# Kernel tuning notes

Measured on AMD Instinct MI355X. Metric: run time of the kernel, lower is better.

Reference implementation:

```python
import jax, jax.numpy as jnp
import numpy as np

KNN = 5
SEARCH = 3
CUTOFF = 1.0
NCLASSES = 21
D, H, W = 32, 128, 2048
P = 1048576


def setup_inputs() -> dict:
    key = jax.random.key(0)
    k1, k2, k3, k4, k5, k6 = jax.random.split(key, 6)
    proj_range = jax.random.uniform(k1, (D, H, W), dtype=jnp.float32)
    unproj_range = jax.random.uniform(k2, (P,), dtype=jnp.float32)
    proj_argmax = jax.random.randint(k3, (D, H, W), 0, NCLASSES).astype(jnp.int32)
    px = jax.random.randint(k4, (P,), 0, W).astype(jnp.int32)
    py = jax.random.randint(k5, (P,), 0, H).astype(jnp.int32)
    pz = jax.random.randint(k6, (P,), 0, D).astype(jnp.int32)
    return {"proj_range": proj_range, "unproj_range": unproj_range,
            "proj_argmax": proj_argmax, "px": px, "py": py, "pz": pz}


def reference(proj_range, unproj_range, proj_argmax, px, py, pz):
    pad = (SEARCH - 1) // 2
    k3 = SEARCH ** 3
    center = (k3 - 1) // 2  # = 13 for search=3
    n_pts = unproj_range.shape[0]

    # zero padding replicates F.unfold's implicit zero pad (padded entries stay 0,
    # which is NOT mapped to inf by the `< 0` mask, matching the torch code)
    pr_pad = jnp.pad(proj_range, pad)
    pa_pad = jnp.pad(proj_argmax, pad)

    # kernel offsets, flattened in (dz, dy, dx) order like unfoldNd
    offs = jnp.arange(SEARCH, dtype=jnp.int32)
    oz, oy, ox = jnp.meshgrid(offs, offs, offs, indexing="ij")
    oz, oy, ox = oz.reshape(-1), oy.reshape(-1), ox.reshape(-1)  # [k3]

    # per-point neighborhood indices into the padded volume: [P, k3]
    zi = pz[:, None] + oz[None, :]
    yi = py[:, None] + oy[None, :]
    xi = px[:, None] + ox[None, :]

    nb_rang = pr_pad[zi, yi, xi]                       # [P, k3]
    nb_rang = jnp.where(nb_rang < 0, jnp.inf, nb_rang)
    nb_rang = nb_rang.at[:, center].set(unproj_range)  # center = query range

    k2_dist = jnp.abs(nb_rang - unproj_range[:, None])  # [P, k3]

    neg_top, knn_idx = jax.lax.top_k(-k2_dist, KNN)     # smallest-k distances
    knn_dist = -neg_top                                  # [P, KNN]

    nb_arg = pa_pad[zi, yi, xi]                          # [P, k3] int
    knn_arg = jnp.take_along_axis(nb_arg, knn_idx, axis=1)
    knn_arg = jnp.where(knn_dist > CUTOFF, NCLASSES, knn_arg)  # cutoff -> invalid class

    # scatter-add voting over classes 0..NCLASSES
    counts = jnp.zeros((n_pts, NCLASSES + 1), dtype=proj_range.dtype)
    counts = counts.at[jnp.arange(n_pts, dtype=jnp.int32)[:, None], knn_arg].add(1.0)

    # argmax over classes 1..NCLASSES-1 (drop class 0 and invalid bucket), then +1
    out = jnp.argmax(counts[:, 1:-1], axis=1).astype(jnp.int32) + 1
    return out
```

## Files before the change

kernel.cpp:

```cpp
#include <hip/hip_runtime.h>
#include <math.h>

#define KNN 5
#define K3 27
#define CENTER 13
#define NCLASSES 21
#define DIM_D 32
#define DIM_H 128
#define DIM_W 2048

#define RADIX 256
#define BIN_PTS 2048
#define SEG_TILE 2048


typedef float    float4u __attribute__((ext_vector_type(4), aligned(4)));
typedef int      int4u   __attribute__((ext_vector_type(4), aligned(4)));
typedef unsigned uint4u  __attribute__((ext_vector_type(4), aligned(4)));

#define SENTINEL 3.0e38f
#define BITS_TWO 0x4000000000000000ULL
#define M_SCALE 8388608.0f

__device__ __forceinline__ unsigned seg_of_xy(int x, int y) {
    return ((unsigned)y << 1) | ((unsigned)x >> 10);
}
__device__ __forceinline__ unsigned seg_of_wy(unsigned wy) {
    return (((wy >> 11) & 0x7Fu) << 1) | ((wy >> 10) & 1u);
}
__device__ __forceinline__ unsigned b8_of_wy(unsigned wy) {
    return (((wy >> 18) & 31u) << 3) | ((wy >> 7) & 7u);
}

__global__ __launch_bounds__(256) void pack_hist_kernel(
    const float4* __restrict__ pr4, const int4* __restrict__ pa4,
    uint4* __restrict__ cv4,
    const int* __restrict__ px, const int* __restrict__ py,
    unsigned* __restrict__ partial, int n4, int P, int chunk)
{
    __shared__ unsigned lh0[RADIX];
    int t = threadIdx.x, b = blockIdx.x;

    int i = b * 256 + t;
    if (i < n4) {
        float4 v = pr4[i];
        int4   c = pa4[i];
        uint4 w;
        w.x = ((unsigned)(v.x * M_SCALE) << 5) | ((unsigned)c.x & 31u);
        w.y = ((unsigned)(v.y * M_SCALE) << 5) | ((unsigned)c.y & 31u);
        w.z = ((unsigned)(v.z * M_SCALE) << 5) | ((unsigned)c.z & 31u);
        w.w = ((unsigned)(v.w * M_SCALE) << 5) | ((unsigned)c.w & 31u);
        cv4[i] = w;
    }

    if (b < RADIX) {
        lh0[t] = 0;
        __syncthreads();
        int start = b * chunk;
        int end = min(P, start + chunk);
        for (int i0 = start + t * 4; i0 < end; i0 += 256 * 4) {
            if (i0 + 3 < end) {
                int i4 = i0 >> 2;
                int4 X = ((const int4*)px)[i4];
                int4 Y = ((const int4*)py)[i4];
                atomicAdd(&lh0[seg_of_xy(X.x, Y.x)], 1u);
                atomicAdd(&lh0[seg_of_xy(X.y, Y.y)], 1u);
                atomicAdd(&lh0[seg_of_xy(X.z, Y.z)], 1u);
                atomicAdd(&lh0[seg_of_xy(X.w, Y.w)], 1u);
            } else {
                for (int j = i0; j < end; ++j)
                    atomicAdd(&lh0[seg_of_xy(px[j], py[j])], 1u);
            }
        }
        __syncthreads();
        partial[b * RADIX + t] = lh0[t];
    }
}

__global__ __launch_bounds__(256) void scan_reduce_kernel(
    const unsigned* __restrict__ partial, unsigned* __restrict__ g0,
    unsigned* __restrict__ hbase)
{
    __shared__ unsigned ws[4];
    int t = threadIdx.x, lane = t & 63, wid = t >> 6;
    unsigned a = 0;
    for (int b = 0; b < RADIX; ++b)
        a += partial[b * RADIX + t];
    unsigned ia = a;
#pragma unroll
    for (int off = 1; off < 64; off <<= 1) {
        unsigned v = __shfl_up(ia, off);
        if (lane >= off) ia += v;
    }
    if (lane == 63) ws[wid] = ia;
    __syncthreads();
    unsigned b = 0;
#pragma unroll
    for (int w = 0; w < 4; ++w) b += (w < wid) ? ws[w] : 0u;
    unsigned excl = b + ia - a;
    g0[t] = excl;
    hbase[t] = excl;
}

struct BinShared {
    unsigned lh[RADIX];
    unsigned lscan[RADIX];
    unsigned gbase[RADIX];
    unsigned wsum[4];
    unsigned stW[BIN_PTS];
    unsigned stU[BIN_PTS];
    unsigned stI[BIN_PTS];
};

__global__ __launch_bounds__(512) void bin_pass1_kernel(
    const float* __restrict__ ur, const int* __restrict__ px,
    const int* __restrict__ py, const int* __restrict__ pz,
    unsigned* __restrict__ g0,
    unsigned* __restrict__ oW, unsigned* __restrict__ oU,
    unsigned* __restrict__ oI, int P)
{
    __shared__ BinShared S;
    int t = threadIdx.x, lane = t & 63, wid = t >> 6;
    int bstart = blockIdx.x * BIN_PTS;
    int n = min(BIN_PTS, P - bstart);
    if (t < RADIX) S.lh[t] = 0;
    __syncthreads();

    unsigned pw[4], pu[4], rk[4], dg[4];
    {
        int i4 = (bstart >> 2) + t;
        int i0 = i4 * 4;
        if (i0 + 3 < P) {
            int4 X = ((const int4*)px)[i4];
            int4 Y = ((const int4*)py)[i4];
            int4 Z = ((const int4*)pz)[i4];
            float4 U = ((const float4*)ur)[i4];
            int xs[4] = {X.x, X.y, X.z, X.w};
            int ys[4] = {Y.x, Y.y, Y.z, Y.w};
            int zs[4] = {Z.x, Z.y, Z.z, Z.w};
            float us[4] = {U.x, U.y, U.z, U.w};
#pragma unroll
            for (int c = 0; c < 4; ++c) {
                dg[c] = seg_of_xy(xs[c], ys[c]);
                rk[c] = atomicAdd(&S.lh[dg[c]], 1u);
                pw[c] = (unsigned)xs[c] | ((unsigned)ys[c] << 11)
                        | ((unsigned)zs[c] << 18);
                pu[c] = (unsigned)(us[c] * M_SCALE);
            }
        } else {
#pragma unroll
            for (int c = 0; c < 4; ++c) {
                int gi = i0 + c;
                if (gi < P) {
                    int x = px[gi], y = py[gi], z = pz[gi];
                    dg[c] = seg_of_xy(x, y);
                    rk[c] = atomicAdd(&S.lh[dg[c]], 1u);
                    pw[c] = (unsigned)x | ((unsigned)y << 11)
                            | ((unsigned)z << 18);
                    pu[c] = (unsigned)(ur[gi] * M_SCALE);
                } else {
                    dg[c] = 0xFFFFFFFFu;
                }
            }
        }
    }
    __syncthreads();

    {
        unsigned c0 = (t < RADIX) ? S.lh[t] : 0u;
        unsigned inc = c0;
#pragma unroll
        for (int off = 1; off < 64; off <<= 1) {
            unsigned v = __shfl_up(inc, off);
            if (lane >= off) inc += v;
        }
        if (t < RADIX && lane == 63) S.wsum[wid] = inc;
        __syncthreads();
        if (t < RADIX) {
            unsigned wb = 0;
#pragma unroll
            for (int w = 0; w < 4; ++w) wb += (w < wid) ? S.wsum[w] : 0u;
            S.lscan[t] = wb + inc - c0;
            S.gbase[t] = c0 ? atomicAdd(&g0[t], c0) : 0u;
        }
    }
    __syncthreads();
#pragma unroll
    for (int c = 0; c < 4; ++c)
        if (dg[c] != 0xFFFFFFFFu) {
            unsigned sl = S.lscan[dg[c]] + rk[c];
            S.stW[sl] = pw[c];
            S.stU[sl] = pu[c];
            S.stI[sl] = (unsigned)(((bstart >> 2) + t) * 4 + c);
        }
    __syncthreads();
#pragma unroll
    for (int j = 0; j < 4; ++j) {
        int s = j * 512 + t;
        if (s < n) {
            unsigned wv = S.stW[s];
            unsigned d = seg_of_wy(wv);
            unsigned pos = S.gbase[d] + ((unsigned)s - S.lscan[d]);
            oW[pos] = wv;
            oU[pos] = S.stU[s];
            oI[pos] = S.stI[s];
        }
    }
}

__device__ __forceinline__ void bev_knn_body_u24(
    const unsigned* __restrict__ cv,
    unsigned mu, int x, int y, int z, int oidx, int* __restrict__ out)
{
    int xo = min(max(x - 1, 0), DIM_W - 4);
    int s = x - 1 - xo;

    uint4u Wv[9];
    bool okr[9];
#pragma unroll
    for (int r = 0; r < 9; ++r) {
        const int dz = r / 3 - 1;
        const int dy = r % 3 - 1;
        int zz = z + dz, yy = y + dy;
        bool ok = ((unsigned)zz < (unsigned)DIM_D) &
                  ((unsigned)yy < (unsigned)DIM_H);
        okr[r] = ok;
        int row = ok ? (zz * DIM_H + yy) : 0;
        Wv[r] = *(const uint4u*)(cv + (((size_t)row) << 11) + xo);
    }

    double bd[KNN];
#pragma unroll
    for (int j = 0; j < KNN; ++j) bd[j] = 1.0e308;

    auto push = [&](int k, unsigned w) {
        int diff = abs((int)(w >> 5) - (int)mu);
        if (k == CENTER) diff = 0;
        double kd = (double)diff * 1024.0
                  + (double)(((unsigned)k << 5) | (w & 31u));
#pragma unroll
        for (int j = 0; j < KNN; ++j) {
            double lo = fmin(bd[j], kd);
            kd = fmax(bd[j], kd);
            bd[j] = lo;
        }
    };

    bool fast = __all(s == 0);
    if (fast) {
#pragma unroll
        for (int r = 0; r < 9; ++r) {
            bool ok = okr[r];
            push(r * 3 + 0, ok ? Wv[r].x : 0u);
            push(r * 3 + 1, ok ? Wv[r].y : 0u);
            push(r * 3 + 2, ok ? Wv[r].z : 0u);
        }
    } else {
#pragma unroll
        for (int r = 0; r < 9; ++r) {
            bool ok = okr[r];
            unsigned a0 = ok ? Wv[r].x : 0u;
            unsigned a1 = ok ? Wv[r].y : 0u;
            unsigned a2 = ok ? Wv[r].z : 0u;
            unsigned a3 = ok ? Wv[r].w : 0u;
            unsigned w0 = (s == 0) ? a0 : ((s == -1) ? 0u : ((s == 1) ? a1 : a2));
            unsigned w1 = (s == 0) ? a1 : ((s == -1) ? a0 : ((s == 1) ? a2 : a3));
            unsigned w2 = (s == 0) ? a2 : ((s == -1) ? a1 : ((s == 1) ? a3 : 0u));
            push(r * 3 + 0, w0);
            push(r * 3 + 1, w1);
            push(r * 3 + 2, w2);
        }
    }

    int votes[KNN];
#pragma unroll
    for (int j = 0; j < KNN; ++j)
        votes[j] = (int)(((unsigned long long)bd[j]) & 31u);

    int best_cnt = 0, best_cls = 1;
#pragma unroll
    for (int j = 0; j < KNN; ++j) {
        int v = votes[j];
        if (v >= 1 && v <= NCLASSES - 1) {
            int cnt = 0;
#pragma unroll
            for (int i = 0; i < KNN; ++i) cnt += (votes[i] == v) ? 1 : 0;
            if (cnt > best_cnt || (cnt == best_cnt && v < best_cls)) {
                best_cnt = cnt;
                best_cls = v;
            }
        }
    }
    __builtin_nontemporal_store(best_cls, &out[oidx]);
}

__global__ __launch_bounds__(1024) void pass2_knn_kernel(
    const unsigned* __restrict__ iW, const unsigned* __restrict__ iU,
    const unsigned* __restrict__ iI, const unsigned* __restrict__ segBase,
    const unsigned* __restrict__ cv, int* __restrict__ out, int P)
{
    __shared__ unsigned lz[RADIX];
    __shared__ unsigned lsc[RADIX];
    __shared__ unsigned wsum[4];
    __shared__ unsigned stW[SEG_TILE];
    __shared__ unsigned stU[SEG_TILE];
    __shared__ unsigned stI[SEG_TILE];

    int bid = blockIdx.x;
    int b = bid >> 1, half = bid & 1;
    unsigned s0 = segBase[b];
    unsigned s1 = (b == RADIX - 1) ? (unsigned)P : segBase[b + 1];
    int t = threadIdx.x, lane = t & 63, wid = t >> 6;

    for (unsigned tb = s0 + (unsigned)half * SEG_TILE; tb < s1;
         tb += 2u * SEG_TILE) {
        unsigned m = min((unsigned)SEG_TILE, s1 - tb);
        if (t < RADIX) lz[t] = 0;
        __syncthreads();
        unsigned vw[2], vu[2], vi[2], rk[2], zz[2];
#pragma unroll
        for (int j = 0; j < 2; ++j) {
            int s = j * 1024 + t;
            if (s < (int)m) {
                unsigned gi = tb + (unsigned)s;
                vw[j] = iW[gi];
                vu[j] = iU[gi];
                vi[j] = iI[gi];
                zz[j] = b8_of_wy(vw[j]);
                rk[j] = atomicAdd(&lz[zz[j]], 1u);
            } else {
                zz[j] = 0xFFFFFFFFu;
            }
        }
        __syncthreads();
        {
            unsigned c0 = (t < RADIX) ? lz[t] : 0u;
            unsigned inc = c0;
#pragma unroll
            for (int off = 1; off < 64; off <<= 1) {
                unsigned v = __shfl_up(inc, off);
                if (lane >= off) inc += v;
            }
            if (t < RADIX && lane == 63) wsum[wid] = inc;
            __syncthreads();
            if (t < RADIX) {
                unsigned wb = 0;
#pragma unroll
                for (int w = 0; w < 4; ++w) wb += (w < wid) ? wsum[w] : 0u;
                lsc[t] = wb + inc - c0;
            }
        }
        __syncthreads();
#pragma unroll
        for (int j = 0; j < 2; ++j)
            if (zz[j] != 0xFFFFFFFFu) {
                unsigned sl = lsc[zz[j]] + rk[j];
                stW[sl] = vw[j];
                stU[sl] = vu[j];
                stI[sl] = vi[j];
            }
        __syncthreads();
#pragma unroll
        for (int j = 0; j < 2; ++j) {
            int sp = j * 1024 + t;
            if (sp < (int)m) {
                unsigned wv = stW[sp];
                int x = (int)(wv & 0x7FFu);
                int y = (int)((wv >> 11) & 0x7Fu);
                int z = (int)((wv >> 18) & 0x1Fu);
                bev_knn_body_u24(cv, stU[sp], x, y, z, (int)stI[sp], out);
            }
        }
        __syncthreads();
    }
}

__device__ __forceinline__ void bev_knn_body_gen(
    const float* __restrict__ pr, const int* __restrict__ pa,
    float u, int x, int y, int z, int oidx, int* __restrict__ out)
{
    int xo = min(max(x - 1, 0), DIM_W - 4);
    int s = x - 1 - xo;

    float4u L[9];
    int4u   A[9];
    bool okr[9];
#pragma unroll
    for (int r = 0; r < 9; ++r) {
        const int dz = r / 3 - 1;
        const int dy = r % 3 - 1;
        int zz = z + dz, yy = y + dy;
        bool ok = ((unsigned)zz < (unsigned)DIM_D) &
                  ((unsigned)yy < (unsigned)DIM_H);
        okr[r] = ok;
        int row = ok ? (zz * DIM_H + yy) : 0;
        size_t rb = ((size_t)row) << 11;
        L[r] = *(const float4u*)(pr + rb + xo);
        A[r] = *(const int4u*)(pa + rb + xo);
    }

    double bd[KNN];
#pragma unroll
    for (int j = 0; j < KNN; ++j) bd[j] = 1.0e308;

    auto push = [&](int k, float v, unsigned cls) {
        float d = fabsf(v - u);
        d = (v < 0.f) ? SENTINEL : d;
        if (k == CENTER) d = 0.0f;
        double key = (double)d + 1.0;
        unsigned long long kb =
            (unsigned long long)__double_as_longlong(key)
            | (unsigned long long)(((unsigned)k << 5) | (cls & 31u));
        double kd = __longlong_as_double((long long)kb);
#pragma unroll
        for (int j = 0; j < KNN; ++j) {
            double lo = fmin(bd[j], kd);
            kd = fmax(bd[j], kd);
            bd[j] = lo;
        }
    };

#pragma unroll
    for (int r = 0; r < 9; ++r) {
        bool ok = okr[r];
        float a0 = ok ? L[r].x : 0.f;
        float a1 = ok ? L[r].y : 0.f;
        float a2 = ok ? L[r].z : 0.f;
        float a3 = ok ? L[r].w : 0.f;
        float v0 = (s == 0) ? a0 : ((s == -1) ? 0.f : ((s == 1) ? a1 : a2));
        float v1 = (s == 0) ? a1 : ((s == -1) ? a0 : ((s == 1) ? a2 : a3));
        float v2 = (s == 0) ? a2 : ((s == -1) ? a1 : ((s == 1) ? a3 : 0.f));
        unsigned c0 = ok ? (unsigned)A[r].x : 0u;
        unsigned c1 = ok ? (unsigned)A[r].y : 0u;
        unsigned c2 = ok ? (unsigned)A[r].z : 0u;
        unsigned c3 = ok ? (unsigned)A[r].w : 0u;
        unsigned cv0 = (s == 0) ? c0 : ((s == -1) ? 0u : ((s == 1) ? c1 : c2));
        unsigned cv1 = (s == 0) ? c1 : ((s == -1) ? c0 : ((s == 1) ? c2 : c3));
        unsigned cv2 = (s == 0) ? c2 : ((s == -1) ? c1 : ((s == 1) ? c3 : 0u));
        push(r * 3 + 0, v0, cv0);
        push(r * 3 + 1, v1, cv1);
        push(r * 3 + 2, v2, cv2);
    }

    int votes[KNN];
#pragma unroll
    for (int j = 0; j < KNN; ++j) {
        unsigned long long kb =
            (unsigned long long)__double_as_longlong(bd[j]);
        int cls = (int)(kb & 31u);
        bool cut = (kb & ~1023ULL) > BITS_TWO;
        votes[j] = cut ? NCLASSES : cls;
    }

    int best_cnt = 0, best_cls = 1;
#pragma unroll
    for (int j = 0; j < KNN; ++j) {
        int v = votes[j];
        if (v >= 1 && v <= NCLASSES - 1) {
            int cnt = 0;
#pragma unroll
            for (int i = 0; i < KNN; ++i) cnt += (votes[i] == v) ? 1 : 0;
            if (cnt > best_cnt || (cnt == best_cnt && v < best_cls)) {
                best_cnt = cnt;
                best_cls = v;
            }
        }
    }
    out[oidx] = best_cls;
}

__global__ __launch_bounds__(256) void bev_knn_direct_kernel(
    const float* __restrict__ pr, const int* __restrict__ pa,
    const float* __restrict__ ur, const int* __restrict__ px,
    const int* __restrict__ py, const int* __restrict__ pz,
    int* __restrict__ out, int P)
{
    int p = blockIdx.x * blockDim.x + threadIdx.x;
    if (p >= P) return;
    bev_knn_body_gen(pr, pa, ur[p], px[p], py[p], pz[p], p, out);
}

extern "C" void kernel_launch(void* const* d_in, const int* in_sizes, int n_in,
                              void* d_out, int out_size, void* d_ws, size_t ws_size,
                              hipStream_t stream) {
    const float* pr = (const float*)d_in[0];
    const float* ur = (const float*)d_in[1];
    const int*   pa = (const int*)d_in[2];
    const int*   px = (const int*)d_in[3];
    const int*   py = (const int*)d_in[4];
    const int*   pz = (const int*)d_in[5];
    int* out = (int*)d_out;
    int P = in_sizes[1];
    int gridB = (P + BIN_PTS - 1) / BIN_PTS;
    int gridD = (P + 255) / 256;
    int chunk = (((P + RADIX - 1) / RADIX) + 3) & ~3;

    const int VOXELS = DIM_D * DIM_H * DIM_W;
    size_t g0_b   = (size_t)RADIX * 4;
    size_t hb_b   = (size_t)RADIX * 4;
    size_t part_b = (size_t)RADIX * RADIX * 4;
    size_t pre    = (g0_b + hb_b + part_b + 255) & ~(size_t)255;
    size_t arr_b  = ((size_t)P * 4 + 255) & ~(size_t)255;
    size_t cv_b   = ((size_t)VOXELS * 4 + 255) & ~(size_t)255;
    size_t need   = pre + 3 * arr_b + cv_b;

    if (ws_size >= need) {
        char* ws = (char*)d_ws;
        unsigned* g0     = (unsigned*)ws;
        unsigned* h0base = (unsigned*)(ws + g0_b);
        unsigned* part   = (unsigned*)(ws + g0_b + hb_b);
        unsigned* p1W = (unsigned*)(ws + pre);
        unsigned* p1U = (unsigned*)(ws + pre + arr_b);
        unsigned* p1I = (unsigned*)(ws + pre + 2 * arr_b);
        unsigned* cv  = (unsigned*)(ws + pre + 3 * arr_b);

        int n4 = VOXELS / 4;
        int gridP = max((n4 + 255) / 256, RADIX);
        pack_hist_kernel<<<gridP, 256, 0, stream>>>(
            (const float4*)pr, (const int4*)pa, (uint4*)cv,
            px, py, part, n4, P, chunk);
        scan_reduce_kernel<<<1, 256, 0, stream>>>(part, g0, h0base);
        bin_pass1_kernel<<<gridB, 512, 0, stream>>>(ur, px, py, pz, g0,
                                                    p1W, p1U, p1I, P);
        pass2_knn_kernel<<<2 * RADIX, 1024, 0, stream>>>(
            p1W, p1U, p1I, h0base, cv, out, P);
    } else {
        bev_knn_direct_kernel<<<gridD, 256, 0, stream>>>(pr, pa, ur, px, py,
                                                         pz, out, P);
    }
}
```

Baseline: 191.2 us.

## Split pass2 into fixed 1024-point windows with XCD-aware block swizzle

Pass 2 no longer has 512 blocks each looping over tiles of a variable-size segment. It now launches one block per fixed 1024-point window of the binned arrays, which removes the per-segment base array and balances load across blocks. A block-index swizzle spreads neighbouring windows across the 8 XCDs. Windows that straddle segment boundaries still get a local 8-bit radix sort, so sort locality may drop slightly at the edges, and each block now does a single small tile, which adds launch and sync overhead per point.

```diff
diff --git a/kernel.cpp b/kernel.cpp
--- a/kernel.cpp
+++ b/kernel.cpp
@@ -11,7 +11,7 @@
 
 #define RADIX 256
 #define BIN_PTS 2048
-#define SEG_TILE 2048
+#define WIN 1024
 
 
 typedef float    float4u __attribute__((ext_vector_type(4), aligned(4)));
@@ -78,8 +78,7 @@
 }
 
 __global__ __launch_bounds__(256) void scan_reduce_kernel(
-    const unsigned* __restrict__ partial, unsigned* __restrict__ g0,
-    unsigned* __restrict__ hbase)
+    const unsigned* __restrict__ partial, unsigned* __restrict__ g0)
 {
     __shared__ unsigned ws[4];
     int t = threadIdx.x, lane = t & 63, wid = t >> 6;
@@ -97,9 +96,7 @@
     unsigned b = 0;
 #pragma unroll
     for (int w = 0; w < 4; ++w) b += (w < wid) ? ws[w] : 0u;
-    unsigned excl = b + ia - a;
-    g0[t] = excl;
-    hbase[t] = excl;
+    g0[t] = b + ia - a;
 }
 
 struct BinShared {
@@ -294,84 +291,74 @@
     __builtin_nontemporal_store(best_cls, &out[oidx]);
 }
 
+__device__ __forceinline__ int swizzle_block(int b, int nb) {
+    if ((nb & 7) == 0) {
+        int per = nb >> 3;
+        return (b & 7) * per + (b >> 3);
+    }
+    return b;
+}
+
 __global__ __launch_bounds__(1024) void pass2_knn_kernel(
     const unsigned* __restrict__ iW, const unsigned* __restrict__ iU,
-    const unsigned* __restrict__ iI, const unsigned* __restrict__ segBase,
+    const unsigned* __restrict__ iI,
     const unsigned* __restrict__ cv, int* __restrict__ out, int P)
 {
     __shared__ unsigned lz[RADIX];
     __shared__ unsigned lsc[RADIX];
     __shared__ unsigned wsum[4];
-    __shared__ unsigned stW[SEG_TILE];
-    __shared__ unsigned stU[SEG_TILE];
-    __shared__ unsigned stI[SEG_TILE];
-
-    int bid = blockIdx.x;
-    int b = bid >> 1, half = bid & 1;
-    unsigned s0 = segBase[b];
-    unsigned s1 = (b == RADIX - 1) ? (unsigned)P : segBase[b + 1];
+    __shared__ unsigned stW[WIN];
+    __shared__ unsigned stU[WIN];
+    __shared__ unsigned stI[WIN];
+
+    int lb = swizzle_block(blockIdx.x, gridDim.x);
+    int base = lb * WIN;
+    int m = min(WIN, P - base);
     int t = threadIdx.x, lane = t & 63, wid = t >> 6;
 
-    for (unsigned tb = s0 + (unsigned)half * SEG_TILE; tb < s1;
-         tb += 2u * SEG_TILE) {
-        unsigned m = min((unsigned)SEG_TILE, s1 - tb);
-        if (t < RADIX) lz[t] = 0;
+    if (t < RADIX) lz[t] = 0;
+    __syncthreads();
+
+    unsigned vw = 0, vu = 0, vi = 0, rk = 0, zz = 0xFFFFFFFFu;
+    if (t < m) {
+        vw = iW[base + t];
+        vu = iU[base + t];
+        vi = iI[base + t];
+        zz = b8_of_wy(vw);
+        rk = atomicAdd(&lz[zz], 1u);
+    }
+    __syncthreads();
+    {
+        unsigned c0 = (t < RADIX) ? lz[t] : 0u;
+        unsigned inc = c0;
+#pragma unroll
+        for (int off = 1; off < 64; off <<= 1) {
+            unsigned v = __shfl_up(inc, off);
+            if (lane >= off) inc += v;
+        }
+        if (t < RADIX && lane == 63) wsum[wid] = inc;
         __syncthreads();
-        unsigned vw[2], vu[2], vi[2], rk[2], zz[2];
-#pragma unroll
-        for (int j = 0; j < 2; ++j) {
-            int s = j * 1024 + t;
-            if (s < (int)m) {
-                unsigned gi = tb + (unsigned)s;
-                vw[j] = iW[gi];
-                vu[j] = iU[gi];
-                vi[j] = iI[gi];
-                zz[j] = b8_of_wy(vw[j]);
-                rk[j] = atomicAdd(&lz[zz[j]], 1u);
-            } else {
-                zz[j] = 0xFFFFFFFFu;
-            }
-        }
-        __syncthreads();
-        {
-            unsigned c0 = (t < RADIX) ? lz[t] : 0u;
-            unsigned inc = c0;
-#pragma unroll
-            for (int off = 1; off < 64; off <<= 1) {
-                unsigned v = __shfl_up(inc, off);
-                if (lane >= off) inc += v;
-            }
-            if (t < RADIX && lane == 63) wsum[wid] = inc;
-            __syncthreads();
-            if (t < RADIX) {
-                unsigned wb = 0;
-#pragma unroll
-                for (int w = 0; w < 4; ++w) wb += (w < wid) ? wsum[w] : 0u;
-                lsc[t] = wb + inc - c0;
-            }
-        }
-        __syncthreads();
-#pragma unroll
-        for (int j = 0; j < 2; ++j)
-            if (zz[j] != 0xFFFFFFFFu) {
-                unsigned sl = lsc[zz[j]] + rk[j];
-                stW[sl] = vw[j];
-                stU[sl] = vu[j];
-                stI[sl] = vi[j];
-            }
-        __syncthreads();
-#pragma unroll
-        for (int j = 0; j < 2; ++j) {
-            int sp = j * 1024 + t;
-            if (sp < (int)m) {
-                unsigned wv = stW[sp];
-                int x = (int)(wv & 0x7FFu);
-                int y = (int)((wv >> 11) & 0x7Fu);
-                int z = (int)((wv >> 18) & 0x1Fu);
-                bev_knn_body_u24(cv, stU[sp], x, y, z, (int)stI[sp], out);
-            }
-        }
-        __syncthreads();
+        if (t < RADIX) {
+            unsigned wb = 0;
+#pragma unroll
+            for (int w = 0; w < 4; ++w) wb += (w < wid) ? wsum[w] : 0u;
+            lsc[t] = wb + inc - c0;
+        }
+    }
+    __syncthreads();
+    if (zz != 0xFFFFFFFFu) {
+        unsigned sl = lsc[zz] + rk;
+        stW[sl] = vw;
+        stU[sl] = vu;
+        stI[sl] = vi;
+    }
+    __syncthreads();
+    if (t < m) {
+        unsigned wv = stW[t];
+        int x = (int)(wv & 0x7FFu);
+        int y = (int)((wv >> 11) & 0x7Fu);
+        int z = (int)((wv >> 18) & 0x1Fu);
+        bev_knn_body_u24(cv, stU[t], x, y, z, (int)stI[t], out);
     }
 }
 
@@ -493,37 +480,36 @@
     int P = in_sizes[1];
     int gridB = (P + BIN_PTS - 1) / BIN_PTS;
     int gridD = (P + 255) / 256;
+    int gridW = (P + WIN - 1) / WIN;
     int chunk = (((P + RADIX - 1) / RADIX) + 3) & ~3;
 
     const int VOXELS = DIM_D * DIM_H * DIM_W;
     size_t g0_b   = (size_t)RADIX * 4;
-    size_t hb_b   = (size_t)RADIX * 4;
     size_t part_b = (size_t)RADIX * RADIX * 4;
-    size_t pre    = (g0_b + hb_b + part_b + 255) & ~(size_t)255;
+    size_t pre    = (g0_b + part_b + 255) & ~(size_t)255;
     size_t arr_b  = ((size_t)P * 4 + 255) & ~(size_t)255;
     size_t cv_b   = ((size_t)VOXELS * 4 + 255) & ~(size_t)255;
     size_t need   = pre + 3 * arr_b + cv_b;
 
     if (ws_size >= need) {
         char* ws = (char*)d_ws;
-        unsigned* g0     = (unsigned*)ws;
-        unsigned* h0base = (unsigned*)(ws + g0_b);
-        unsigned* part   = (unsigned*)(ws + g0_b + hb_b);
-        unsigned* p1W = (unsigned*)(ws + pre);
-        unsigned* p1U = (unsigned*)(ws + pre + arr_b);
-        unsigned* p1I = (unsigned*)(ws + pre + 2 * arr_b);
-        unsigned* cv  = (unsigned*)(ws + pre + 3 * arr_b);
+        unsigned* g0   = (unsigned*)ws;
+        unsigned* part = (unsigned*)(ws + g0_b);
+        unsigned* p1W  = (unsigned*)(ws + pre);
+        unsigned* p1U  = (unsigned*)(ws + pre + arr_b);
+        unsigned* p1I  = (unsigned*)(ws + pre + 2 * arr_b);
+        unsigned* cv   = (unsigned*)(ws + pre + 3 * arr_b);
 
         int n4 = VOXELS / 4;
         int gridP = max((n4 + 255) / 256, RADIX);
         pack_hist_kernel<<<gridP, 256, 0, stream>>>(
             (const float4*)pr, (const int4*)pa, (uint4*)cv,
             px, py, part, n4, P, chunk);
-        scan_reduce_kernel<<<1, 256, 0, stream>>>(part, g0, h0base);
+        scan_reduce_kernel<<<1, 256, 0, stream>>>(part, g0);
         bin_pass1_kernel<<<gridB, 512, 0, stream>>>(ur, px, py, pz, g0,
                                                     p1W, p1U, p1I, P);
-        pass2_knn_kernel<<<2 * RADIX, 1024, 0, stream>>>(
-            p1W, p1U, p1I, h0base, cv, out, P);
+        pass2_knn_kernel<<<gridW, 1024, 0, stream>>>(
+            p1W, p1U, p1I, cv, out, P);
     } else {
         bev_knn_direct_kernel<<<gridD, 256, 0, stream>>>(pr, pa, ur, px, py,
                                                          pz, out, P);
```

Result: faster. 183.8 us (-3.9%).
